# Performance work log

Measured on AMD Instinct MI355X. Metric: run time of the kernel, lower is better.

The kernel has to match this reference:

```python
import jax, jax.numpy as jnp
import numpy as np

TEMPERATURE = 0.07
BASE_TEMPERATURE = 0.07
TOP_K = 15  # epoch=0 branch of the original forward


def _pairwise_dist(a, b):
    # a: [M, D], b: [N, D] -> [M, N] euclidean distance (same math as
    # torch.norm(a.unsqueeze(1) - b.unsqueeze(0), dim=2)), safe at 0.
    sq = (jnp.sum(a * a, axis=-1)[:, None]
          + jnp.sum(b * b, axis=-1)[None, :]
          - 2.0 * (a @ b.T))
    sq = jnp.maximum(sq, 0.0)
    pos = sq > 0.0
    return jnp.where(pos, jnp.sqrt(jnp.where(pos, sq, 1.0)), 0.0)


def setup_inputs() -> dict:
    key = jax.random.key(0)
    k1, k2, k3, k4 = jax.random.split(key, 4)
    B, V, D, N, KMAX = 512, 2, 128, 100000, 50
    features = jax.random.normal(k1, (B, V, D), dtype=jnp.float32)
    saved_features = jax.random.normal(k2, (N, D), dtype=jnp.float32)
    indices = jax.random.randint(k3, (B,), 0, N)
    rks = jax.random.randint(k4, (N, KMAX), 0, N)
    return {"features": features, "indices": indices,
            "saved_features": saved_features, "rks": rks}


def reference(features, indices, saved_features, rks):
    B, V, D = features.shape
    M = V * B
    # torch.cat(torch.unbind(features, dim=1), dim=0)
    contrast = jnp.swapaxes(features, 0, 1).reshape(M, D)
    anchor = contrast  # contrast_mode == 'all'

    d0 = _pairwise_dist(anchor, contrast)                      # [M, M]
    adc_orig = (1.0 + 1.0 / (1.0 + d0)) / TEMPERATURE

    # neighbors_features: mat_k = saved_features[rks[indices, k]], duplicated
    neigh = saved_features[rks[indices, :TOP_K]]               # [B, K, D]
    mats = jnp.swapaxes(neigh, 0, 1)                           # [K, B, D]
    mats = jnp.concatenate([mats, mats], axis=1)               # [K, M, D]

    dk = jax.vmap(lambda m: _pairwise_dist(anchor, m))(mats)   # [K, M, M]
    adck = (1.0 + 1.0 / (1.0 + dk)) / TEMPERATURE

    # p_const = 1 -> plain mean over k; sym accumulation is the transpose
    acc = jnp.sum(adck, axis=0) / TOP_K
    acc_sym = acc.T

    summed = acc ** 2 + acc_sym ** 2 + adc_orig ** 2
    logits_src = jnp.sqrt(summed)  # summed >= adc_orig^2 > 0, sqrt is safe

    logits_max = jax.lax.stop_gradient(jnp.max(logits_src, axis=1, keepdims=True))
    logits = logits_src - logits_max

    mask = jnp.tile(jnp.eye(B, dtype=jnp.float32), (V, V))     # [M, M]
    logits_mask = 1.0 - jnp.eye(M, dtype=jnp.float32)
    mask = mask * logits_mask

    exp_logits = jnp.exp(logits) * logits_mask
    log_prob = logits - jnp.log(jnp.sum(exp_logits, axis=1, keepdims=True))

    mask_pos_pairs = jnp.sum(mask, axis=1)
    mask_pos_pairs = jnp.where(mask_pos_pairs < 1e-6, 1.0, mask_pos_pairs)
    mean_log_prob_pos = jnp.sum(mask * log_prob, axis=1) / mask_pos_pairs

    loss = -(TEMPERATURE / BASE_TEMPERATURE) * mean_log_prob_pos
    return jnp.mean(loss.reshape(V, B))
```

## Files before the change

### kernel.cpp

```cpp
#include <hip/hip_runtime.h>
#include <math.h>

#define BB 512
#define VV 2
#define MM 1024
#define DD 128
#define KMAX 50
#define TOPK 15
#define INV_T (1.0f/0.07f)

#define OFF_ANCH  0
#define OFF_A2    262144
#define OFF_ACCT  266240
#define OFF_PART  (266240 + 2097152)
#define OFF_LSPOS (OFF_PART + 65536)

typedef __attribute__((ext_vector_type(8))) short bf16x8;
typedef __attribute__((ext_vector_type(4))) float f32x4;

__device__ __forceinline__ short f2bf(float x)
{
    union { float f; unsigned u; } a; a.f = x;
    return (short)((a.u + 0x7FFFu + ((a.u >> 16) & 1u)) >> 16);
}

__device__ __forceinline__ bf16x8 cvt8(float4 p0, float4 p1, float& nacc)
{
    float v[8] = {p0.x, p0.y, p0.z, p0.w, p1.x, p1.y, p1.z, p1.w};
    bf16x8 r;
    #pragma unroll
    for (int e = 0; e < 8; ++e) {
        nacc = fmaf(v[e], v[e], nacc);
        r[e] = f2bf(v[e]);
    }
    return r;
}

__global__ __launch_bounds__(256) void k0_anchor(
    const float* __restrict__ feat,
    unsigned* __restrict__ anchor_u,
    float* __restrict__ a2)
{
    const int row  = blockIdx.x * 4 + (threadIdx.x >> 6);
    const int lane = threadIdx.x & 63;
    const int frow = (row & (BB - 1)) * VV + (row >> 9);
    float2 v = *(const float2*)&feat[(size_t)frow * DD + lane * 2];
    unsigned lo = (unsigned)(unsigned short)f2bf(v.x);
    unsigned hi = (unsigned)(unsigned short)f2bf(v.y);
    anchor_u[row * (DD / 2) + lane] = lo | (hi << 16);
    float sq = v.x * v.x + v.y * v.y;
    #pragma unroll
    for (int off = 32; off > 0; off >>= 1) sq += __shfl_xor(sq, off);
    if (lane == 0) a2[row] = sq;
}

__global__ __launch_bounds__(256) void k1_acc(
    const short* __restrict__ anchor,
    const float* __restrict__ a2,
    const int* __restrict__ indices,
    const float* __restrict__ saved, const int* __restrict__ rks,
    float* __restrict__ accT)
{
    const int tid = threadIdx.x;
    const int lane = tid & 63;
    const int wid = tid >> 6;
    const int lr = lane & 15;
    const int lg = lane >> 4;
    const int wr = wid >> 1;
    const int wc = wid & 1;
    const int m0 = blockIdx.x * 64 + wr * 32;

    int aidx[2];
    #pragma unroll
    for (int tm = 0; tm < 2; ++tm) {
        int b = (m0 >> 4) + tm;
        aidx[tm] = rks[(size_t)indices[b] * KMAX + lr];
    }
    bf16x8 af[2][4];
    float nnA[2] = {0.f, 0.f};
    #pragma unroll
    for (int tm = 0; tm < 2; ++tm)
        #pragma unroll
        for (int kc = 0; kc < 4; ++kc) {
            const float4* p = (const float4*)&saved[(size_t)aidx[tm] * DD + kc * 32 + lg * 8];
            af[tm][kc] = cvt8(p[0], p[1], nnA[tm]);
        }
    #pragma unroll
    for (int tm = 0; tm < 2; ++tm) {
        nnA[tm] += __shfl_xor(nnA[tm], 16);
        nnA[tm] += __shfl_xor(nnA[tm], 32);
    }
    float nnAr[2][4];
    #pragma unroll
    for (int tm = 0; tm < 2; ++tm)
        #pragma unroll
        for (int r = 0; r < 4; ++r)
            nnAr[tm][r] = __shfl(nnA[tm], lg * 4 + r);

    #pragma unroll
    for (int jt = 0; jt < 2; ++jt) {
        const int j0 = blockIdx.y * 256 + jt * 128 + wc * 64;
        f32x4 acc[2][4];
        #pragma unroll
        for (int a = 0; a < 2; ++a)
            #pragma unroll
            for (int b = 0; b < 4; ++b) acc[a][b] = (f32x4){0.f, 0.f, 0.f, 0.f};
        #pragma unroll
        for (int kc = 0; kc < 4; ++kc) {
            bf16x8 bf[4];
            #pragma unroll
            for (int tn = 0; tn < 4; ++tn)
                bf[tn] = *(const bf16x8*)&anchor[(size_t)(j0 + tn * 16 + lr) * DD + kc * 32 + lg * 8];
            #pragma unroll
            for (int tm = 0; tm < 2; ++tm)
                #pragma unroll
                for (int tn = 0; tn < 4; ++tn)
                    acc[tm][tn] = __builtin_amdgcn_mfma_f32_16x16x32_bf16(
                        af[tm][kc], bf[tn], acc[tm][tn], 0, 0, 0);
        }
        #pragma unroll
        for (int tm = 0; tm < 2; ++tm) {
            const int b = (m0 >> 4) + tm;
            #pragma unroll
            for (int tn = 0; tn < 4; ++tn) {
                const float a2j = a2[j0 + tn * 16 + lr];
                float s = 0.f;
                #pragma unroll
                for (int r = 0; r < 4; ++r) {
                    float g = acc[tm][tn][r];
                    float sq = fmaxf(fmaf(-2.f, g, a2j + nnAr[tm][r]), 0.f);
                    float d = __builtin_amdgcn_sqrtf(sq);
                    float f = fmaf(__builtin_amdgcn_rcpf(1.f + d), INV_T, INV_T);
                    if (lg == 3 && r == 3) f = 0.f;
                    s += f;
                }
                s += __shfl_xor(s, 16);
                s += __shfl_xor(s, 32);
                if (lane < 16)
                    accT[(size_t)b * MM + j0 + tn * 16 + lane] = s * (1.0f / TOPK);
            }
        }
    }
}

__global__ __launch_bounds__(256) void k2_exp(
    const short* __restrict__ anchor, const float* __restrict__ a2,
    const float* __restrict__ accT,
    float* __restrict__ part, float* __restrict__ lspos)
{
    __shared__ float pshare[4][16];
    const int tid = threadIdx.x;
    const int lane = tid & 63;
    const int wid = tid >> 6;
    const int lr = lane & 15;
    const int lg = lane >> 4;
    const int i0 = blockIdx.x * 16;
    const int jg = blockIdx.y;
    const int jcol = jg * 64 + wid * 16 + lr;

    f32x4 acc = (f32x4){0.f, 0.f, 0.f, 0.f};
    #pragma unroll
    for (int kc = 0; kc < 4; ++kc) {
        bf16x8 af = *(const bf16x8*)&anchor[(size_t)(i0 + lr) * DD + kc * 32 + lg * 8];
        bf16x8 bf = *(const bf16x8*)&anchor[(size_t)jcol * DD + kc * 32 + lg * 8];
        acc = __builtin_amdgcn_mfma_f32_16x16x32_bf16(af, bf, acc, 0, 0, 0);
    }
    const int ib4 = i0 + lg * 4;
    const float4 a2i4 = *(const float4*)&a2[ib4];
    const float a2iv[4] = {a2i4.x, a2i4.y, a2i4.z, a2i4.w};
    const float a2j = a2[jcol];
    const float4 aij4 = *(const float4*)&accT[(size_t)(jcol & (BB - 1)) * MM + ib4];
    const float aijv[4] = {aij4.x, aij4.y, aij4.z, aij4.w};

    float esum[4];
    #pragma unroll
    for (int r = 0; r < 4; ++r) {
        const int i = ib4 + r;
        float g = acc[r];
        float sq = fmaxf(fmaf(-2.f, g, a2iv[r] + a2j), 0.f);
        float d0 = __builtin_amdgcn_sqrtf(sq);
        float adc = fmaf(__builtin_amdgcn_rcpf(1.f + d0), INV_T, INV_T);
        float aji = accT[(size_t)(i & (BB - 1)) * MM + jcol];
        float ls = __builtin_amdgcn_sqrtf(aijv[r] * aijv[r] + aji * aji + adc * adc);
        esum[r] = (jcol == i) ? 0.f : __expf(ls);
        if (jcol == (i ^ BB)) lspos[i] = ls;
    }
    #pragma unroll
    for (int r = 0; r < 4; ++r) {
        float e = esum[r];
        e += __shfl_xor(e, 1);
        e += __shfl_xor(e, 2);
        e += __shfl_xor(e, 4);
        e += __shfl_xor(e, 8);
        if (lr == 0) pshare[wid][lg * 4 + r] = e;
    }
    __syncthreads();
    if (tid < 16)
        part[jg * MM + i0 + tid] =
            pshare[0][tid] + pshare[1][tid] + pshare[2][tid] + pshare[3][tid];
}

__global__ __launch_bounds__(256) void k3_finish(
    const float* __restrict__ part, const float* __restrict__ lspos,
    float* __restrict__ out)
{
    __shared__ float red[4];
    const int tid = threadIdx.x;
    const int lane = tid & 63, w = tid >> 6;
    float lsum = 0.f;
    #pragma unroll
    for (int q = 0; q < 4; ++q) {
        const int i = tid + q * 256;
        float s = 0.f;
        #pragma unroll
        for (int jg = 0; jg < 16; ++jg) s += part[jg * MM + i];
        lsum += __logf(s) - lspos[i];
    }
    #pragma unroll
    for (int off = 32; off > 0; off >>= 1) lsum += __shfl_xor(lsum, off);
    if (lane == 0) red[w] = lsum;
    __syncthreads();
    if (tid == 0) out[0] = (red[0] + red[1] + red[2] + red[3]) * (1.0f / MM);
}

extern "C" void kernel_launch(void* const* d_in, const int* in_sizes, int n_in,
                              void* d_out, int out_size, void* d_ws, size_t ws_size,
                              hipStream_t stream)
{
    const float* feat    = (const float*)d_in[0];
    const int*   indices = (const int*)  d_in[1];
    const float* saved   = (const float*)d_in[2];
    const int*   rks     = (const int*)  d_in[3];

    char* w = (char*)d_ws;
    short* anchor = (short*)(w + OFF_ANCH);
    float* a2     = (float*)(w + OFF_A2);
    float* accT   = (float*)(w + OFF_ACCT);
    float* part   = (float*)(w + OFF_PART);
    float* lspos  = (float*)(w + OFF_LSPOS);

    k0_anchor<<<MM / 4, 256, 0, stream>>>(feat, (unsigned*)anchor, a2);
    k1_acc<<<dim3(128, 4), 256, 0, stream>>>(anchor, a2, indices, saved, rks, accT);
    k2_exp<<<dim3(64, 16), 256, 0, stream>>>(anchor, a2, accT, part, lspos);
    k3_finish<<<1, 256, 0, stream>>>(part, lspos, (float*)d_out);
}
```

Baseline: 35.70 us.

## Fuse finish kernel into exp kernel via atomics and last-block reduction

Removes the separate single-block finish kernel. The exp kernel now atomically accumulates row sums and positive logits, and the last block to finish, found through an atomic counter, computes the final loss. The accumulator kernel is also remapped to one block per batch sample with each wave covering 256 columns, which removes the duplicated neighbour gathers across the column-split grid. This saves one launch, but it adds float atomics (nondeterministic summation order) and a zeroing step in the anchor kernel.

```diff
diff --git a/kernel.cpp b/kernel.cpp
--- a/kernel.cpp
+++ b/kernel.cpp
@@ -9,11 +9,12 @@
 #define TOPK 15
 #define INV_T (1.0f/0.07f)
 
-#define OFF_ANCH  0
-#define OFF_A2    262144
-#define OFF_ACCT  266240
-#define OFF_PART  (266240 + 2097152)
-#define OFF_LSPOS (OFF_PART + 65536)
+#define OFF_ANCH   0
+#define OFF_A2     262144
+#define OFF_ACCT   266240
+#define OFF_ROWSUM 2363392
+#define OFF_POSSUM 2367488
+#define OFF_CNT    2367744
 
 typedef __attribute__((ext_vector_type(8))) short bf16x8;
 typedef __attribute__((ext_vector_type(4))) float f32x4;
@@ -39,10 +40,13 @@
 __global__ __launch_bounds__(256) void k0_anchor(
     const float* __restrict__ feat,
     unsigned* __restrict__ anchor_u,
-    float* __restrict__ a2)
-{
-    const int row  = blockIdx.x * 4 + (threadIdx.x >> 6);
-    const int lane = threadIdx.x & 63;
+    float* __restrict__ a2,
+    float* __restrict__ rowsum, float* __restrict__ possum,
+    unsigned* __restrict__ cnt)
+{
+    const int tid  = threadIdx.x;
+    const int row  = blockIdx.x * 4 + (tid >> 6);
+    const int lane = tid & 63;
     const int frow = (row & (BB - 1)) * VV + (row >> 9);
     float2 v = *(const float2*)&feat[(size_t)frow * DD + lane * 2];
     unsigned lo = (unsigned)(unsigned short)f2bf(v.x);
@@ -52,6 +56,13 @@
     #pragma unroll
     for (int off = 32; off > 0; off >>= 1) sq += __shfl_xor(sq, off);
     if (lane == 0) a2[row] = sq;
+
+    if (blockIdx.x == 0) {
+        #pragma unroll
+        for (int q = 0; q < 4; ++q) rowsum[tid + q * 256] = 0.f;
+        if (tid < 64) possum[tid] = 0.f;
+        if (tid == 0) *cnt = 0u;
+    }
 }
 
 __global__ __launch_bounds__(256) void k1_acc(
@@ -66,45 +77,30 @@
     const int wid = tid >> 6;
     const int lr = lane & 15;
     const int lg = lane >> 4;
-    const int wr = wid >> 1;
-    const int wc = wid & 1;
-    const int m0 = blockIdx.x * 64 + wr * 32;
-
-    int aidx[2];
-    #pragma unroll
-    for (int tm = 0; tm < 2; ++tm) {
-        int b = (m0 >> 4) + tm;
-        aidx[tm] = rks[(size_t)indices[b] * KMAX + lr];
-    }
-    bf16x8 af[2][4];
-    float nnA[2] = {0.f, 0.f};
-    #pragma unroll
-    for (int tm = 0; tm < 2; ++tm)
-        #pragma unroll
-        for (int kc = 0; kc < 4; ++kc) {
-            const float4* p = (const float4*)&saved[(size_t)aidx[tm] * DD + kc * 32 + lg * 8];
-            af[tm][kc] = cvt8(p[0], p[1], nnA[tm]);
-        }
-    #pragma unroll
-    for (int tm = 0; tm < 2; ++tm) {
-        nnA[tm] += __shfl_xor(nnA[tm], 16);
-        nnA[tm] += __shfl_xor(nnA[tm], 32);
-    }
-    float nnAr[2][4];
-    #pragma unroll
-    for (int tm = 0; tm < 2; ++tm)
-        #pragma unroll
-        for (int r = 0; r < 4; ++r)
-            nnAr[tm][r] = __shfl(nnA[tm], lg * 4 + r);
-
-    #pragma unroll
-    for (int jt = 0; jt < 2; ++jt) {
-        const int j0 = blockIdx.y * 256 + jt * 128 + wc * 64;
-        f32x4 acc[2][4];
-        #pragma unroll
-        for (int a = 0; a < 2; ++a)
-            #pragma unroll
-            for (int b = 0; b < 4; ++b) acc[a][b] = (f32x4){0.f, 0.f, 0.f, 0.f};
+    const int b = blockIdx.x;
+
+    const int aidx = rks[(size_t)indices[b] * KMAX + lr];
+
+    bf16x8 af[4];
+    float nnA = 0.f;
+    #pragma unroll
+    for (int kc = 0; kc < 4; ++kc) {
+        const float4* p = (const float4*)&saved[(size_t)aidx * DD + kc * 32 + lg * 8];
+        af[kc] = cvt8(p[0], p[1], nnA);
+    }
+    nnA += __shfl_xor(nnA, 16);
+    nnA += __shfl_xor(nnA, 32);
+    float nnAr[4];
+    #pragma unroll
+    for (int r = 0; r < 4; ++r)
+        nnAr[r] = __shfl(nnA, lg * 4 + r);
+
+    #pragma unroll
+    for (int jt = 0; jt < 4; ++jt) {
+        const int j0 = wid * 256 + jt * 64;
+        f32x4 acc[4];
+        #pragma unroll
+        for (int t = 0; t < 4; ++t) acc[t] = (f32x4){0.f, 0.f, 0.f, 0.f};
         #pragma unroll
         for (int kc = 0; kc < 4; ++kc) {
             bf16x8 bf[4];
@@ -112,33 +108,27 @@
             for (int tn = 0; tn < 4; ++tn)
                 bf[tn] = *(const bf16x8*)&anchor[(size_t)(j0 + tn * 16 + lr) * DD + kc * 32 + lg * 8];
             #pragma unroll
-            for (int tm = 0; tm < 2; ++tm)
-                #pragma unroll
-                for (int tn = 0; tn < 4; ++tn)
-                    acc[tm][tn] = __builtin_amdgcn_mfma_f32_16x16x32_bf16(
-                        af[tm][kc], bf[tn], acc[tm][tn], 0, 0, 0);
+            for (int tn = 0; tn < 4; ++tn)
+                acc[tn] = __builtin_amdgcn_mfma_f32_16x16x32_bf16(
+                    af[kc], bf[tn], acc[tn], 0, 0, 0);
         }
         #pragma unroll
-        for (int tm = 0; tm < 2; ++tm) {
-            const int b = (m0 >> 4) + tm;
+        for (int tn = 0; tn < 4; ++tn) {
+            const float a2j = a2[j0 + tn * 16 + lr];
+            float s = 0.f;
             #pragma unroll
-            for (int tn = 0; tn < 4; ++tn) {
-                const float a2j = a2[j0 + tn * 16 + lr];
-                float s = 0.f;
-                #pragma unroll
-                for (int r = 0; r < 4; ++r) {
-                    float g = acc[tm][tn][r];
-                    float sq = fmaxf(fmaf(-2.f, g, a2j + nnAr[tm][r]), 0.f);
-                    float d = __builtin_amdgcn_sqrtf(sq);
-                    float f = fmaf(__builtin_amdgcn_rcpf(1.f + d), INV_T, INV_T);
-                    if (lg == 3 && r == 3) f = 0.f;
-                    s += f;
-                }
-                s += __shfl_xor(s, 16);
-                s += __shfl_xor(s, 32);
-                if (lane < 16)
-                    accT[(size_t)b * MM + j0 + tn * 16 + lane] = s * (1.0f / TOPK);
+            for (int r = 0; r < 4; ++r) {
+                float g = acc[tn][r];
+                float sq = fmaxf(fmaf(-2.f, g, a2j + nnAr[r]), 0.f);
+                float d = __builtin_amdgcn_sqrtf(sq);
+                float f = fmaf(__builtin_amdgcn_rcpf(1.f + d), INV_T, INV_T);
+                if (lg == 3 && r == 3) f = 0.f;
+                s += f;
             }
+            s += __shfl_xor(s, 16);
+            s += __shfl_xor(s, 32);
+            if (lane < 16)
+                accT[(size_t)b * MM + j0 + tn * 16 + lane] = s * (1.0f / TOPK);
         }
     }
 }
@@ -146,9 +136,12 @@
 __global__ __launch_bounds__(256) void k2_exp(
     const short* __restrict__ anchor, const float* __restrict__ a2,
     const float* __restrict__ accT,
-    float* __restrict__ part, float* __restrict__ lspos)
+    float* __restrict__ rowsum, float* __restrict__ possum,
+    unsigned* __restrict__ cnt, float* __restrict__ out)
 {
     __shared__ float pshare[4][16];
+    __shared__ float red[4];
+    __shared__ int iswin;
     const int tid = threadIdx.x;
     const int lane = tid & 63;
     const int wid = tid >> 6;
@@ -183,7 +176,7 @@
         float aji = accT[(size_t)(i & (BB - 1)) * MM + jcol];
         float ls = __builtin_amdgcn_sqrtf(aijv[r] * aijv[r] + aji * aji + adc * adc);
         esum[r] = (jcol == i) ? 0.f : __expf(ls);
-        if (jcol == (i ^ BB)) lspos[i] = ls;
+        if (jcol == (i ^ BB)) atomicAdd(&possum[i & 63], ls);
     }
     #pragma unroll
     for (int r = 0; r < 4; ++r) {
@@ -196,31 +189,34 @@
     }
     __syncthreads();
     if (tid < 16)
-        part[jg * MM + i0 + tid] =
-            pshare[0][tid] + pshare[1][tid] + pshare[2][tid] + pshare[3][tid];
-}
-
-__global__ __launch_bounds__(256) void k3_finish(
-    const float* __restrict__ part, const float* __restrict__ lspos,
-    float* __restrict__ out)
-{
-    __shared__ float red[4];
-    const int tid = threadIdx.x;
-    const int lane = tid & 63, w = tid >> 6;
+        atomicAdd(&rowsum[i0 + tid],
+                  pshare[0][tid] + pshare[1][tid] + pshare[2][tid] + pshare[3][tid]);
+    __syncthreads();
+    if (tid == 0) {
+        unsigned old = __hip_atomic_fetch_add(cnt, 1u, __ATOMIC_ACQ_REL,
+                                              __HIP_MEMORY_SCOPE_AGENT);
+        iswin = (old == 64u * 16u - 1u);
+    }
+    __syncthreads();
+    if (!iswin) return;
+
     float lsum = 0.f;
     #pragma unroll
     for (int q = 0; q < 4; ++q) {
         const int i = tid + q * 256;
-        float s = 0.f;
-        #pragma unroll
-        for (int jg = 0; jg < 16; ++jg) s += part[jg * MM + i];
-        lsum += __logf(s) - lspos[i];
-    }
+        float rs = __hip_atomic_load(&rowsum[i], __ATOMIC_RELAXED,
+                                     __HIP_MEMORY_SCOPE_AGENT);
+        lsum += __logf(rs);
+    }
+    if (tid < 64)
+        lsum -= __hip_atomic_load(&possum[tid], __ATOMIC_RELAXED,
+                                  __HIP_MEMORY_SCOPE_AGENT);
     #pragma unroll
     for (int off = 32; off > 0; off >>= 1) lsum += __shfl_xor(lsum, off);
-    if (lane == 0) red[w] = lsum;
-    __syncthreads();
-    if (tid == 0) out[0] = (red[0] + red[1] + red[2] + red[3]) * (1.0f / MM);
+    if (lane == 0) red[wid] = lsum;
+    __syncthreads();
+    if (tid == 0)
+        out[0] = (red[0] + red[1] + red[2] + red[3]) * (1.0f / MM);
 }
 
 extern "C" void kernel_launch(void* const* d_in, const int* in_sizes, int n_in,
@@ -233,14 +229,16 @@
     const int*   rks     = (const int*)  d_in[3];
 
     char* w = (char*)d_ws;
-    short* anchor = (short*)(w + OFF_ANCH);
-    float* a2     = (float*)(w + OFF_A2);
-    float* accT   = (float*)(w + OFF_ACCT);
-    float* part   = (float*)(w + OFF_PART);
-    float* lspos  = (float*)(w + OFF_LSPOS);
-
-    k0_anchor<<<MM / 4, 256, 0, stream>>>(feat, (unsigned*)anchor, a2);
-    k1_acc<<<dim3(128, 4), 256, 0, stream>>>(anchor, a2, indices, saved, rks, accT);
-    k2_exp<<<dim3(64, 16), 256, 0, stream>>>(anchor, a2, accT, part, lspos);
-    k3_finish<<<1, 256, 0, stream>>>(part, lspos, (float*)d_out);
-}
+    short*    anchor = (short*)   (w + OFF_ANCH);
+    float*    a2     = (float*)   (w + OFF_A2);
+    float*    accT   = (float*)   (w + OFF_ACCT);
+    float*    rowsum = (float*)   (w + OFF_ROWSUM);
+    float*    possum = (float*)   (w + OFF_POSSUM);
+    unsigned* cnt    = (unsigned*)(w + OFF_CNT);
+
+    k0_anchor<<<MM / 4, 256, 0, stream>>>(feat, (unsigned*)anchor, a2,
+                                          rowsum, possum, cnt);
+    k1_acc<<<BB, 256, 0, stream>>>(anchor, a2, indices, saved, rks, accT);
+    k2_exp<<<dim3(64, 16), 256, 0, stream>>>(anchor, a2, accT,
+                                             rowsum, possum, cnt, (float*)d_out);
+}
```

Result: slower. 58.58 us (+64.1%).

## Fuse anchor conversion into accumulation kernel, recomputing bf16 tiles from features

Applied to the files above, without the earlier changes.

Merges the anchor bf16-conversion kernel and the neighbor-accumulation kernel into a single launch. The conversion runs in the first 256 blocks and the accumulation in the rest. The accumulation blocks no longer read the converted anchor; they load fp32 features directly, convert them to bf16 in registers, and compute the squared norms themselves. This removes one kernel launch and the dependency between the two stages, at the cost of redundant fp32 loads and conversions in every accumulation block.

```diff
diff --git a/kernel.cpp b/kernel.cpp
--- a/kernel.cpp
+++ b/kernel.cpp
@@ -36,39 +36,44 @@
     return r;
 }
 
-__global__ __launch_bounds__(256) void k0_anchor(
-    const float* __restrict__ feat,
-    unsigned* __restrict__ anchor_u,
-    float* __restrict__ a2)
-{
-    const int row  = blockIdx.x * 4 + (threadIdx.x >> 6);
-    const int lane = threadIdx.x & 63;
-    const int frow = (row & (BB - 1)) * VV + (row >> 9);
-    float2 v = *(const float2*)&feat[(size_t)frow * DD + lane * 2];
-    unsigned lo = (unsigned)(unsigned short)f2bf(v.x);
-    unsigned hi = (unsigned)(unsigned short)f2bf(v.y);
-    anchor_u[row * (DD / 2) + lane] = lo | (hi << 16);
-    float sq = v.x * v.x + v.y * v.y;
-    #pragma unroll
-    for (int off = 32; off > 0; off >>= 1) sq += __shfl_xor(sq, off);
-    if (lane == 0) a2[row] = sq;
-}
-
-__global__ __launch_bounds__(256) void k1_acc(
-    const short* __restrict__ anchor,
-    const float* __restrict__ a2,
-    const int* __restrict__ indices,
+__device__ __forceinline__ const float4* feat_ptr(const float* feat, int j, int d)
+{
+    int frow = (j & (BB - 1)) * VV + (j >> 9);
+    return (const float4*)&feat[(size_t)frow * DD + d];
+}
+
+__global__ __launch_bounds__(256) void kA(
+    const float* __restrict__ feat, const int* __restrict__ indices,
     const float* __restrict__ saved, const int* __restrict__ rks,
+    unsigned* __restrict__ anchor_u, float* __restrict__ a2,
     float* __restrict__ accT)
 {
     const int tid = threadIdx.x;
     const int lane = tid & 63;
+
+    if (blockIdx.x < 256) {
+        const int row  = blockIdx.x * 4 + (tid >> 6);
+        const int frow = (row & (BB - 1)) * VV + (row >> 9);
+        float2 v = *(const float2*)&feat[(size_t)frow * DD + lane * 2];
+        unsigned lo = (unsigned)(unsigned short)f2bf(v.x);
+        unsigned hi = (unsigned)(unsigned short)f2bf(v.y);
+        anchor_u[row * (DD / 2) + lane] = lo | (hi << 16);
+        float sq = v.x * v.x + v.y * v.y;
+        #pragma unroll
+        for (int off = 32; off > 0; off >>= 1) sq += __shfl_xor(sq, off);
+        if (lane == 0) a2[row] = sq;
+        return;
+    }
+
+    const int idx = blockIdx.x - 256;
+    const int bx = idx & 127;
+    const int by = idx >> 7;
     const int wid = tid >> 6;
     const int lr = lane & 15;
     const int lg = lane >> 4;
     const int wr = wid >> 1;
     const int wc = wid & 1;
-    const int m0 = blockIdx.x * 64 + wr * 32;
+    const int m0 = bx * 64 + wr * 32;
 
     int aidx[2];
     #pragma unroll
@@ -99,18 +104,21 @@
 
     #pragma unroll
     for (int jt = 0; jt < 2; ++jt) {
-        const int j0 = blockIdx.y * 256 + jt * 128 + wc * 64;
+        const int j0 = by * 256 + jt * 128 + wc * 64;
         f32x4 acc[2][4];
         #pragma unroll
         for (int a = 0; a < 2; ++a)
             #pragma unroll
             for (int b = 0; b < 4; ++b) acc[a][b] = (f32x4){0.f, 0.f, 0.f, 0.f};
+        float nnB[4] = {0.f, 0.f, 0.f, 0.f};
         #pragma unroll
         for (int kc = 0; kc < 4; ++kc) {
             bf16x8 bf[4];
             #pragma unroll
-            for (int tn = 0; tn < 4; ++tn)
-                bf[tn] = *(const bf16x8*)&anchor[(size_t)(j0 + tn * 16 + lr) * DD + kc * 32 + lg * 8];
+            for (int tn = 0; tn < 4; ++tn) {
+                const float4* p = feat_ptr(feat, j0 + tn * 16 + lr, kc * 32 + lg * 8);
+                bf[tn] = cvt8(p[0], p[1], nnB[tn]);
+            }
             #pragma unroll
             for (int tm = 0; tm < 2; ++tm)
                 #pragma unroll
@@ -119,11 +127,16 @@
                         af[tm][kc], bf[tn], acc[tm][tn], 0, 0, 0);
         }
         #pragma unroll
+        for (int tn = 0; tn < 4; ++tn) {
+            nnB[tn] += __shfl_xor(nnB[tn], 16);
+            nnB[tn] += __shfl_xor(nnB[tn], 32);
+        }
+        #pragma unroll
         for (int tm = 0; tm < 2; ++tm) {
             const int b = (m0 >> 4) + tm;
             #pragma unroll
             for (int tn = 0; tn < 4; ++tn) {
-                const float a2j = a2[j0 + tn * 16 + lr];
+                const float a2j = nnB[tn];
                 float s = 0.f;
                 #pragma unroll
                 for (int r = 0; r < 4; ++r) {
@@ -239,8 +252,8 @@
     float* part   = (float*)(w + OFF_PART);
     float* lspos  = (float*)(w + OFF_LSPOS);
 
-    k0_anchor<<<MM / 4, 256, 0, stream>>>(feat, (unsigned*)anchor, a2);
-    k1_acc<<<dim3(128, 4), 256, 0, stream>>>(anchor, a2, indices, saved, rks, accT);
+    kA<<<768, 256, 0, stream>>>(feat, indices, saved, rks,
+                                (unsigned*)anchor, a2, accT);
     k2_exp<<<dim3(64, 16), 256, 0, stream>>>(anchor, a2, accT, part, lspos);
     k3_finish<<<1, 256, 0, stream>>>(part, lspos, (float*)d_out);
 }
```

New measurement: 36.98 us. +3.6%, slower.

## Exploit symmetry of logits matrix to compute only upper triangle in k2

Applied to the files above, without the earlier changes.

The logits_src matrix is symmetric, so k2 now skips blocks below the diagonal and counts each upper-triangle exp term twice, once as a row partial and once as a column partial. k0 zeroes the partial buffers that skipped blocks would otherwise leave unset, and the finish kernel sums both the row and the column partials. This roughly halves the exp/MFMA work in k2 but adds column-partial writes and a much longer reduction loop in the single-block finish kernel (64 extra loads per row).

```diff
diff --git a/kernel.cpp b/kernel.cpp
--- a/kernel.cpp
+++ b/kernel.cpp
@@ -12,8 +12,9 @@
 #define OFF_ANCH  0
 #define OFF_A2    262144
 #define OFF_ACCT  266240
-#define OFF_PART  (266240 + 2097152)
-#define OFF_LSPOS (OFF_PART + 65536)
+#define OFF_PARTR 2363392
+#define OFF_PARTC 2428928
+#define OFF_LSPOS 2691072
 
 typedef __attribute__((ext_vector_type(8))) short bf16x8;
 typedef __attribute__((ext_vector_type(4))) float f32x4;
@@ -39,7 +40,8 @@
 __global__ __launch_bounds__(256) void k0_anchor(
     const float* __restrict__ feat,
     unsigned* __restrict__ anchor_u,
-    float* __restrict__ a2)
+    float* __restrict__ a2,
+    float4* __restrict__ partzero)
 {
     const int row  = blockIdx.x * 4 + (threadIdx.x >> 6);
     const int lane = threadIdx.x & 63;
@@ -52,6 +54,10 @@
     #pragma unroll
     for (int off = 32; off > 0; off >>= 1) sq += __shfl_xor(sq, off);
     if (lane == 0) a2[row] = sq;
+
+    const int gid = blockIdx.x * 256 + threadIdx.x;
+    if (gid < (320 * 1024 / 16))
+        partzero[gid] = make_float4(0.f, 0.f, 0.f, 0.f);
 }
 
 __global__ __launch_bounds__(256) void k1_acc(
@@ -146,16 +152,20 @@
 __global__ __launch_bounds__(256) void k2_exp(
     const short* __restrict__ anchor, const float* __restrict__ a2,
     const float* __restrict__ accT,
-    float* __restrict__ part, float* __restrict__ lspos)
-{
+    float* __restrict__ partR, float* __restrict__ partC,
+    float* __restrict__ lspos)
+{
+    const int rg = blockIdx.x;
+    const int jg = blockIdx.y;
+    if (jg < (rg >> 2)) return;
+
     __shared__ float pshare[4][16];
     const int tid = threadIdx.x;
     const int lane = tid & 63;
     const int wid = tid >> 6;
     const int lr = lane & 15;
     const int lg = lane >> 4;
-    const int i0 = blockIdx.x * 16;
-    const int jg = blockIdx.y;
+    const int i0 = rg * 16;
     const int jcol = jg * 64 + wid * 16 + lr;
 
     f32x4 acc = (f32x4){0.f, 0.f, 0.f, 0.f};
@@ -172,7 +182,7 @@
     const float4 aij4 = *(const float4*)&accT[(size_t)(jcol & (BB - 1)) * MM + ib4];
     const float aijv[4] = {aij4.x, aij4.y, aij4.z, aij4.w};
 
-    float esum[4];
+    float es[4];
     #pragma unroll
     for (int r = 0; r < 4; ++r) {
         const int i = ib4 + r;
@@ -182,12 +192,18 @@
         float adc = fmaf(__builtin_amdgcn_rcpf(1.f + d0), INV_T, INV_T);
         float aji = accT[(size_t)(i & (BB - 1)) * MM + jcol];
         float ls = __builtin_amdgcn_sqrtf(aijv[r] * aijv[r] + aji * aji + adc * adc);
-        esum[r] = (jcol == i) ? 0.f : __expf(ls);
-        if (jcol == (i ^ BB)) lspos[i] = ls;
-    }
+        es[r] = (jcol > i) ? __expf(ls) : 0.f;
+        if (jcol == (i ^ BB) && jcol > i) lspos[i] = ls;
+    }
+
+    float cs = es[0] + es[1] + es[2] + es[3];
+    cs += __shfl_xor(cs, 16);
+    cs += __shfl_xor(cs, 32);
+    if (lg == 0) partC[(size_t)rg * MM + jcol] = cs;
+
     #pragma unroll
     for (int r = 0; r < 4; ++r) {
-        float e = esum[r];
+        float e = es[r];
         e += __shfl_xor(e, 1);
         e += __shfl_xor(e, 2);
         e += __shfl_xor(e, 4);
@@ -196,13 +212,13 @@
     }
     __syncthreads();
     if (tid < 16)
-        part[jg * MM + i0 + tid] =
+        partR[(size_t)jg * MM + i0 + tid] =
             pshare[0][tid] + pshare[1][tid] + pshare[2][tid] + pshare[3][tid];
 }
 
 __global__ __launch_bounds__(256) void k3_finish(
-    const float* __restrict__ part, const float* __restrict__ lspos,
-    float* __restrict__ out)
+    const float* __restrict__ partR, const float* __restrict__ partC,
+    const float* __restrict__ lspos, float* __restrict__ out)
 {
     __shared__ float red[4];
     const int tid = threadIdx.x;
@@ -213,8 +229,10 @@
         const int i = tid + q * 256;
         float s = 0.f;
         #pragma unroll
-        for (int jg = 0; jg < 16; ++jg) s += part[jg * MM + i];
-        lsum += __logf(s) - lspos[i];
+        for (int jg = 0; jg < 16; ++jg) s += partR[(size_t)jg * MM + i];
+        #pragma unroll
+        for (int rg = 0; rg < 64; ++rg) s += partC[(size_t)rg * MM + i];
+        lsum += __logf(s) - lspos[i & (BB - 1)];
     }
     #pragma unroll
     for (int off = 32; off > 0; off >>= 1) lsum += __shfl_xor(lsum, off);
@@ -236,11 +254,13 @@
     short* anchor = (short*)(w + OFF_ANCH);
     float* a2     = (float*)(w + OFF_A2);
     float* accT   = (float*)(w + OFF_ACCT);
-    float* part   = (float*)(w + OFF_PART);
+    float* partR  = (float*)(w + OFF_PARTR);
+    float* partC  = (float*)(w + OFF_PARTC);
     float* lspos  = (float*)(w + OFF_LSPOS);
 
-    k0_anchor<<<MM / 4, 256, 0, stream>>>(feat, (unsigned*)anchor, a2);
+    k0_anchor<<<MM / 4, 256, 0, stream>>>(feat, (unsigned*)anchor, a2,
+                                          (float4*)partR);
     k1_acc<<<dim3(128, 4), 256, 0, stream>>>(anchor, a2, indices, saved, rks, accT);
-    k2_exp<<<dim3(64, 16), 256, 0, stream>>>(anchor, a2, accT, part, lspos);
-    k3_finish<<<1, 256, 0, stream>>>(part, lspos, (float*)d_out);
-}
+    k2_exp<<<dim3(64, 16), 256, 0, stream>>>(anchor, a2, accT, partR, partC, lspos);
+    k3_finish<<<1, 256, 0, stream>>>(partR, partC, lspos, (float*)d_out);
+}
```

Result: slower. 95.37 us (+167.1%).
